# Performance work log

Hardware: AMD Instinct MI355X
Metric: run time of the kernel (lower is better)

## Reference

```python
import jax, jax.numpy as jnp
import numpy as np

N = 5000
NFEAT = 512
NHID = 64
NHEADS = 8
NCLASS = 40
ALPHA = 0.2  # leaky relu slope
NEG_INF = -9e15


def setup_inputs() -> dict:
    key = jax.random.key(0)
    ks = jax.random.split(key, 12)
    x = jax.random.normal(ks[0], (N, NFEAT), dtype=jnp.float32)
    # binary adjacency, ~32 avg degree, with self loops
    adj = (jax.random.uniform(ks[1], (N, N)) < (32.0 / N)).astype(jnp.float32)
    adj = jnp.maximum(adj, jnp.eye(N, dtype=jnp.float32))
    s = 1.0 / np.sqrt(NFEAT)
    W_h = jax.random.uniform(ks[2], (NHEADS, NFEAT, NHID), minval=-s, maxval=s, dtype=jnp.float32)
    a_h = jax.random.uniform(ks[3], (NHEADS, 2 * NHID), minval=-s, maxval=s, dtype=jnp.float32)
    s2 = 1.0 / np.sqrt(NHID * NHEADS)
    W_o = jax.random.uniform(ks[4], (NHID * NHEADS, NHID), minval=-s2, maxval=s2, dtype=jnp.float32)
    a_o = jax.random.uniform(ks[5], (2 * NHID,), minval=-s2, maxval=s2, dtype=jnp.float32)
    s3 = 1.0 / np.sqrt(NHID)
    fc1_w = jax.random.uniform(ks[6], (NHID, 200), minval=-s3, maxval=s3, dtype=jnp.float32)
    fc1_b = jax.random.uniform(ks[7], (200,), minval=-s3, maxval=s3, dtype=jnp.float32)
    s4 = 1.0 / np.sqrt(200)
    fc2_w = jax.random.uniform(ks[8], (200, NCLASS), minval=-s4, maxval=s4, dtype=jnp.float32)
    fc2_b = jax.random.uniform(ks[9], (NCLASS,), minval=-s4, maxval=s4, dtype=jnp.float32)
    return {"x": x, "adj": adj, "W_h": W_h, "a_h": a_h, "W_o": W_o, "a_o": a_o,
            "fc1_w": fc1_w, "fc1_b": fc1_b, "fc2_w": fc2_w, "fc2_b": fc2_b}


def _masked_attention(e, adj):
    # e: [..., N, N]; mask where adj == 0, then row softmax
    e = jnp.where(adj > 0, e, NEG_INF)
    return jax.nn.softmax(e, axis=-1)


def reference(x, adj, W_h, a_h, W_o, a_o, fc1_w, fc1_b, fc2_w, fc2_b):
    # ---- multi-head GAT layer (concat=True), eval mode (dropout off) ----
    Wh = jnp.einsum('nf,hfo->hno', x, W_h)                 # [H, N, nhid]
    f1 = jnp.einsum('hno,ho->hn', Wh, a_h[:, :NHID])       # [H, N]
    f2 = jnp.einsum('hno,ho->hn', Wh, a_h[:, NHID:])       # [H, N]
    e = jax.nn.leaky_relu(f1[:, :, None] + f2[:, None, :], ALPHA)  # [H, N, N]
    att = _masked_attention(e, adj[None, :, :])
    h = jnp.einsum('hnm,hmo->hno', att, Wh)                # [H, N, nhid]
    h1 = jax.nn.elu(h).transpose(1, 0, 2).reshape(N, NHEADS * NHID)  # concat heads

    # ---- output GAT layer (concat=False) ----
    Wh2 = h1 @ W_o                                         # [N, nhid]
    g1 = Wh2 @ a_o[:NHID]                                  # [N]
    g2 = Wh2 @ a_o[NHID:]                                  # [N]
    e2 = jax.nn.leaky_relu(g1[:, None] + g2[None, :], ALPHA)
    att2 = _masked_attention(e2, adj)
    h2 = att2 @ Wh2                                        # [N, nhid]

    # ---- MLP head ----
    h3 = jax.nn.elu(h2 @ fc1_w + fc1_b)
    return h3 @ fc2_w + fc2_b                              # [N, nclass]
```

## Files before the change

### kernel.cpp

```cpp
#include <hip/hip_runtime.h>

typedef unsigned short u16;
typedef unsigned int u32;
typedef unsigned long long u64;
typedef __bf16 bf16_t;
typedef __bf16 bf16x8 __attribute__((ext_vector_type(8)));
typedef float f32x4 __attribute__((ext_vector_type(4)));
typedef u32 u32x4 __attribute__((ext_vector_type(4)));

#define NN 5000
#define NF 512
#define NH 64
#define HEADS 8
#define NCLS 40
#define CAP 128
#define LRELU 0.2f

#define CVT_BIG 320
#define CVT_GRID (CVT_BIG + 8)
#define BM_BLKS 1250
#define G1_BLKS (79 * HEADS)

__device__ __forceinline__ bool adj_is_bf16(const void* adj) {
    return ((*(const u32*)adj) & 0xFFFFu) != 0u;
}
__device__ __forceinline__ u16 rne_bf16(float f) {
    u32 u = __float_as_uint(f);
    u += 0x7FFFu + ((u >> 16) & 1u);
    return (u16)(u >> 16);
}
__device__ __forceinline__ float up_bf16(u16 h) {
    return __uint_as_float((u32)h << 16);
}
__device__ __forceinline__ u32x4 ntload4(const void* p, int idx) {
    return __builtin_nontemporal_load(((const u32x4*)p) + idx);
}

__global__ __launch_bounds__(256) void cvt(const void* __restrict__ x, const void* __restrict__ W_h,
                                           const void* __restrict__ adj,
                                           const void* a_h, const void* W_o, const void* a_o,
                                           const void* f1w, const void* f1b,
                                           const void* f2w, const void* f2b,
                                           u16* __restrict__ xc, u16* __restrict__ whc,
                                           float* a_hc, float* W_oc, float* a_oc,
                                           float* f1wc, float* f1bc, float* f2wc, float* f2bc) {
    const bool isb = adj_is_bf16(adj);
    const int b = blockIdx.x;
    if (b < CVT_BIG) {
        const int X4 = NN * NF / 4;
        const int T4 = X4 + HEADS * NF * NH / 4;
        for (int i = b * 256 + threadIdx.x; i < T4; i += CVT_BIG * 256) {
            if (i < X4) {
                ushort4 o;
                if (isb) {
                    o = ((const ushort4*)x)[i];
                } else {
                    u32x4 vv = ntload4(x, i);
                    o.x = rne_bf16(__uint_as_float(vv[0])); o.y = rne_bf16(__uint_as_float(vv[1]));
                    o.z = rne_bf16(__uint_as_float(vv[2])); o.w = rne_bf16(__uint_as_float(vv[3]));
                }
                ((ushort4*)xc)[i] = o;
            } else {
                const int iw = i - X4;
                u16 q[4];
                if (isb) {
                    ushort4 vv = ((const ushort4*)W_h)[iw];
                    q[0] = vv.x; q[1] = vv.y; q[2] = vv.z; q[3] = vv.w;
                } else {
                    u32x4 vv = ntload4(W_h, iw);
                    q[0] = rne_bf16(__uint_as_float(vv[0])); q[1] = rne_bf16(__uint_as_float(vv[1]));
                    q[2] = rne_bf16(__uint_as_float(vv[2])); q[3] = rne_bf16(__uint_as_float(vv[3]));
                }
                const int e0 = iw * 4;
                const int h = e0 >> 15;
                const int rem = e0 & 32767;
                const int f = rem >> 6, o0 = rem & 63;
                const int base = (h * 16 + (f >> 5)) * 2048 + ((f >> 3) & 3) * 128 + (f & 7);
                #pragma unroll
                for (int k = 0; k < 4; ++k) {
                    const int o = o0 + k;
                    whc[base + (o >> 4) * 512 + (o & 15) * 8] = q[k];
                }
            }
        }
    } else {
        const int s0 = HEADS * 2 * NH, s1 = HEADS * NH * NH, s2 = 2 * NH,
                  s3 = NH * 200, s4 = 200, s5 = 200 * NCLS, s6 = NCLS;
        const int total = s0 + s1 + s2 + s3 + s4 + s5 + s6;
        for (int i = (b - CVT_BIG) * 256 + threadIdx.x; i < total; i += 8 * 256) {
            const void* src; float* dst; int off = i;
            if (off < s0) { src = a_h; dst = a_hc; }
            else if ((off -= s0) < s1) { src = W_o;  dst = W_oc; }
            else if ((off -= s1) < s2) { src = a_o;  dst = a_oc; }
            else if ((off -= s2) < s3) { src = f1w;  dst = f1wc; }
            else if ((off -= s3) < s4) { src = f1b;  dst = f1bc; }
            else if ((off -= s4) < s5) { src = f2w;  dst = f2wc; }
            else { off -= s5;           src = f2b;  dst = f2bc; }
            dst[off] = isb ? up_bf16(((const u16*)src)[off]) : ((const float*)src)[off];
        }
    }
}

__global__ __launch_bounds__(256) void gemm1_f(const bf16_t* __restrict__ x,
                                               const bf16_t* __restrict__ Wf,
                                               const float* __restrict__ a_h,
                                               const void* __restrict__ adj,
                                               int* __restrict__ nbr, int* __restrict__ deg,
                                               float* __restrict__ Wh,
                                               float* __restrict__ f1,
                                               float* __restrict__ f2) {
    const int lane = threadIdx.x & 63;
    const int wid  = threadIdx.x >> 6;
    const int b = blockIdx.x;

    if (b >= G1_BLKS) {
        const bool isb = adj_is_bf16(adj);
        const int r = (b - G1_BLKS) * 4 + wid;
        u64 my0 = 0ull, my1 = 0ull;
        if (!isb) {
            const float* row = (const float*)adj + (size_t)r * NN;
            #pragma unroll
            for (int pass = 0; pass < 2; ++pass) {
                u32x4 v[10];
                #pragma unroll
                for (int k = 0; k < 10; ++k) {
                    int c = (pass * 10 + k) * 64 + lane;
                    v[k] = (c < 1250) ? ntload4(row, c) : (u32x4){0u, 0u, 0u, 0u};
                }
                #pragma unroll
                for (int k = 0; k < 10; ++k) {
                    int i = pass * 10 + k;
                    #pragma unroll
                    for (int j = 0; j < 4; ++j) {
                        u64 m = __ballot(v[k][j] != 0u);
                        int w = i * 4 + j;
                        if (w == lane)      my0 = m;
                        if (w == lane + 64) my1 = m;
                    }
                }
            }
        } else {
            const u16* row = (const u16*)adj + (size_t)r * NN;
            u32x4 v[10];
            #pragma unroll
            for (int k = 0; k < 10; ++k) {
                int c = k * 64 + lane;
                v[k] = (c < 625) ? ntload4(row, c) : (u32x4){0u, 0u, 0u, 0u};
            }
            #pragma unroll
            for (int k = 0; k < 10; ++k) {
                #pragma unroll
                for (int j = 0; j < 4; ++j) {
                    u64 mlo = __ballot((v[k][j] & 0xFFFFu) != 0u);
                    u64 mhi = __ballot((v[k][j] >> 16) != 0u);
                    int wl = k * 8 + 2 * j, wh = wl + 1;
                    if (wl == lane)      my0 = mlo;
                    if (wl == lane + 64) my1 = mlo;
                    if (wh == lane)      my0 = mhi;
                    if (wh == lane + 64) my1 = mhi;
                }
            }
        }
        int* nrow = nbr + (size_t)r * CAP;
        int pc = __popcll(my0);
        int scan = pc;
        #pragma unroll
        for (int o = 1; o < 64; o <<= 1) {
            int t2 = __shfl_up(scan, o);
            if (lane >= o) scan += t2;
        }
        int off = scan - pc;
        {
            const int w = lane;
            u64 mw = my0;
            while (mw) {
                int bb = __ffsll(mw) - 1;
                mw &= mw - 1;
                int elem = !isb ? ((w >> 2) * 64 + bb) * 4 + (w & 3)
                                : ((w >> 3) * 64 + bb) * 8 + (w & 7);
                if (off < CAP) nrow[off] = elem;
                ++off;
            }
        }
        const int base = __shfl(scan, 63);
        int pc1 = __popcll(my1);
        int scan1 = pc1;
        #pragma unroll
        for (int o = 1; o < 64; o <<= 1) {
            int t2 = __shfl_up(scan1, o);
            if (lane >= o) scan1 += t2;
        }
        int off1 = base + scan1 - pc1;
        {
            const int w = lane + 64;
            u64 mw = my1;
            while (mw) {
                int bb = __ffsll(mw) - 1;
                mw &= mw - 1;
                int elem = !isb ? ((w >> 2) * 64 + bb) * 4 + (w & 3)
                                : ((w >> 3) * 64 + bb) * 8 + (w & 7);
                if (off1 < CAP) nrow[off1] = elem;
                ++off1;
            }
        }
        const int total = base + __shfl(scan1, 63);
        if (lane == 0) deg[r] = total < CAP ? total : CAP;
        return;
    }

    const int rg = b % 79;
    const int h  = b / 79;
    const int quad = lane >> 4;
    const int lr   = lane & 15;
    const int kq   = quad * 8;
    const int nCol = wid * 16 + lr;
    __shared__ float f1s[4][64], f2s[4][64];

    const bf16_t* Bf = Wf + (size_t)h * (16 * 2048) + threadIdx.x * 8;
    bf16x8 bfrag[16];
    #pragma unroll
    for (int s = 0; s < 16; ++s) bfrag[s] = *(const bf16x8*)(Bf + s * 2048);

    const float a1c = a_h[h * 128 + nCol];
    const float a2c = a_h[h * 128 + NH + nCol];

    for (int t = 0; t < 4; ++t) {
        const int rb = rg * 64 + t * 16;
        int row  = rb + lr;
        int rowc = row < NN ? row : NN - 1;
        const bf16_t* xp = x + (size_t)rowc * NF + kq;
        f32x4 acc = {0.f, 0.f, 0.f, 0.f};
        #pragma unroll
        for (int s = 0; s < 16; ++s) {
            bf16x8 a = *(const bf16x8*)(xp + s * 32);
            acc = __builtin_amdgcn_mfma_f32_16x16x32_bf16(a, bfrag[s], acc, 0, 0, 0);
        }
        #pragma unroll
        for (int r = 0; r < 4; ++r) {
            int gr = rb + quad * 4 + r;
            if (gr < NN) Wh[(size_t)gr * (HEADS * NH) + h * NH + nCol] = acc[r];
            float p1 = acc[r] * a1c, p2 = acc[r] * a2c;
            #pragma unroll
            for (int o = 8; o; o >>= 1) { p1 += __shfl_xor(p1, o); p2 += __shfl_xor(p2, o); }
            if (lr == 0) { f1s[wid][t * 16 + quad * 4 + r] = p1; f2s[wid][t * 16 + quad * 4 + r] = p2; }
        }
    }
    __syncthreads();
    if (wid == 0) {
        int gr = rg * 64 + lane;
        if (gr < NN) {
            f1[h * NN + gr] = f1s[0][lane] + f1s[1][lane] + f1s[2][lane] + f1s[3][lane];
            f2[h * NN + gr] = f2s[0][lane] + f2s[1][lane] + f2s[2][lane] + f2s[3][lane];
        }
    }
}

__global__ __launch_bounds__(256) void agg1f(const int* __restrict__ nbr,
                                             const int* __restrict__ deg,
                                             const float* __restrict__ Wh,
                                             const float* __restrict__ f1,
                                             const float* __restrict__ f2,
                                             float* __restrict__ h1) {
    const int lane = threadIdx.x & 63;
    const int wid  = threadIdx.x >> 6;
    const int n = blockIdx.x;
    __shared__ int s_nbr[CAP];
    __shared__ float s_p[8][CAP];
    const int d = deg[n];
    for (int i = threadIdx.x; i < d; i += 256) s_nbr[i] = nbr[(size_t)n * CAP + i];
    __syncthreads();

    const int ha = wid, hb = wid + 4;
    const int nb0 = (lane < d) ? s_nbr[lane] : 0;
    const int nb1 = (lane + 64 < d) ? s_nbr[lane + 64] : 0;
    const float f10 = f1[ha * NN + n], f11 = f1[hb * NN + n];
    const float* f2ha = f2 + (size_t)ha * NN;
    const float* f2hb = f2 + (size_t)hb * NN;

    float e00 = -INFINITY, e01 = -INFINITY, e10 = -INFINITY, e11 = -INFINITY;
    if (lane < d) {
        float a = f10 + f2ha[nb0]; e00 = a > 0.f ? a : LRELU * a;
        float b = f11 + f2hb[nb0]; e10 = b > 0.f ? b : LRELU * b;
    }
    if (lane + 64 < d) {
        float a = f10 + f2ha[nb1]; e01 = a > 0.f ? a : LRELU * a;
        float b = f11 + f2hb[nb1]; e11 = b > 0.f ? b : LRELU * b;
    }
    float mx0 = fmaxf(e00, e01), mx1 = fmaxf(e10, e11);
    #pragma unroll
    for (int o = 32; o; o >>= 1) {
        mx0 = fmaxf(mx0, __shfl_xor(mx0, o));
        mx1 = fmaxf(mx1, __shfl_xor(mx1, o));
    }
    float p00 = lane < d ? expf(e00 - mx0) : 0.f;
    float p01 = lane + 64 < d ? expf(e01 - mx0) : 0.f;
    float p10 = lane < d ? expf(e10 - mx1) : 0.f;
    float p11 = lane + 64 < d ? expf(e11 - mx1) : 0.f;
    float sm0 = p00 + p01, sm1 = p10 + p11;
    #pragma unroll
    for (int o = 32; o; o >>= 1) { sm0 += __shfl_xor(sm0, o); sm1 += __shfl_xor(sm1, o); }

    const float i0 = 1.f / sm0, i1 = 1.f / sm1;
    s_p[ha][lane] = p00 * i0; s_p[ha][lane + 64] = p01 * i0;
    s_p[hb][lane] = p10 * i1; s_p[hb][lane + 64] = p11 * i1;
    __syncthreads();

    const float* ap = s_p[2 * wid + (lane >> 5)];
    const float* wp = Wh + wid * 128 + 2 * lane;
    float A0x = 0.f, A0y = 0.f, A1x = 0.f, A1y = 0.f;
    float A2x = 0.f, A2y = 0.f, A3x = 0.f, A3y = 0.f;
    int j = 0;
    for (; j + 8 <= d; j += 8) {
        #pragma unroll
        for (int u = 0; u < 8; ++u) {
            const float2 v = *(const float2*)(wp + (size_t)s_nbr[j + u] * (HEADS * NH));
            const float a = ap[j + u];
            if ((u & 3) == 0)      { A0x += a * v.x; A0y += a * v.y; }
            else if ((u & 3) == 1) { A1x += a * v.x; A1y += a * v.y; }
            else if ((u & 3) == 2) { A2x += a * v.x; A2y += a * v.y; }
            else                   { A3x += a * v.x; A3y += a * v.y; }
        }
    }
    for (; j < d; ++j) {
        const float2 v = *(const float2*)(wp + (size_t)s_nbr[j] * (HEADS * NH));
        const float a = ap[j];
        A0x += a * v.x; A0y += a * v.y;
    }
    float hx = A0x + A1x + A2x + A3x;
    float hy = A0y + A1y + A2y + A3y;
    hx = hx > 0.f ? hx : expf(hx) - 1.f;
    hy = hy > 0.f ? hy : expf(hy) - 1.f;
    *(float2*)(h1 + (size_t)n * (HEADS * NH) + wid * 128 + 2 * lane) = make_float2(hx, hy);
}

__global__ __launch_bounds__(256) void gemm2_4(const float* __restrict__ h1,
                                               const float* __restrict__ W_o,
                                               const float* __restrict__ a_o,
                                               float* __restrict__ Wh2,
                                               float* __restrict__ g1,
                                               float* __restrict__ g2) {
    const int t = threadIdx.x;
    const int n0 = blockIdx.x * 4;
    __shared__ float sh[4 * 512];
    __shared__ float ps[4][4][64];
    const float4* src = (const float4*)(h1 + (size_t)n0 * 512);
    ((float4*)sh)[t]       = src[t];
    ((float4*)sh)[t + 256] = src[t + 256];
    __syncthreads();
    const int o = t & 63, part = t >> 6;
    float a0 = 0.f, a1 = 0.f, a2 = 0.f, a3 = 0.f;
    const float* wo = W_o + part * 128 * 64 + o;
    const float* s0 = sh + part * 128;
    #pragma unroll 4
    for (int f = 0; f < 128; ++f) {
        float w = wo[f * 64];
        a0 += s0[f] * w; a1 += s0[512 + f] * w; a2 += s0[1024 + f] * w; a3 += s0[1536 + f] * w;
    }
    ps[part][0][o] = a0; ps[part][1][o] = a1; ps[part][2][o] = a2; ps[part][3][o] = a3;
    __syncthreads();
    const int nd = t >> 6;
    float w2 = ps[0][nd][o] + ps[1][nd][o] + ps[2][nd][o] + ps[3][nd][o];
    Wh2[(size_t)(n0 + nd) * 64 + o] = w2;
    float p1 = w2 * a_o[o], p2 = w2 * a_o[64 + o];
    #pragma unroll
    for (int s = 32; s; s >>= 1) { p1 += __shfl_xor(p1, s); p2 += __shfl_xor(p2, s); }
    if (o == 0) { g1[n0 + nd] = p1; g2[n0 + nd] = p2; }
}

__global__ __launch_bounds__(256) void agg2_mlp(const float* __restrict__ Wh2,
                                                const float* __restrict__ g1,
                                                const float* __restrict__ g2,
                                                const int* __restrict__ nbr,
                                                const int* __restrict__ deg,
                                                const float* __restrict__ fc1_w,
                                                const float* __restrict__ fc1_b,
                                                const float* __restrict__ fc2_w,
                                                const float* __restrict__ fc2_b,
                                                float* __restrict__ out) {
    const int lane = threadIdx.x & 63;
    const int wid  = threadIdx.x >> 6;
    const int t = threadIdx.x;
    const int n0 = blockIdx.x * 4;
    const int n = n0 + wid;
    __shared__ float s_alpha[4][CAP];
    __shared__ int   s_nbr[4][CAP];
    __shared__ float s_h2[4][NH];
    __shared__ float s_h3[4][200];
    __shared__ float ps2[2][4][NCLS];
    const int d = deg[n];
    const int* nb = nbr + (size_t)n * CAP;
    const float gn = g1[n];

    float mx = -INFINITY;
    for (int j = lane; j < d; j += 64) {
        int m = nb[j];
        s_nbr[wid][j] = m;
        float e = gn + g2[m];
        e = e > 0.f ? e : LRELU * e;
        s_alpha[wid][j] = e;
        mx = fmaxf(mx, e);
    }
    #pragma unroll
    for (int o = 32; o; o >>= 1) mx = fmaxf(mx, __shfl_xor(mx, o));
    float sm = 0.f;
    for (int j = lane; j < d; j += 64) {
        float p = expf(s_alpha[wid][j] - mx);
        s_alpha[wid][j] = p;
        sm += p;
    }
    #pragma unroll
    for (int o = 32; o; o >>= 1) sm += __shfl_xor(sm, o);

    float acc0 = 0.f, acc1 = 0.f, acc2 = 0.f, acc3 = 0.f;
    int j = 0;
    for (; j + 4 <= d; j += 4) {
        acc0 += s_alpha[wid][j]     * Wh2[(size_t)s_nbr[wid][j]     * NH + lane];
        acc1 += s_alpha[wid][j + 1] * Wh2[(size_t)s_nbr[wid][j + 1] * NH + lane];
        acc2 += s_alpha[wid][j + 2] * Wh2[(size_t)s_nbr[wid][j + 2] * NH + lane];
        acc3 += s_alpha[wid][j + 3] * Wh2[(size_t)s_nbr[wid][j + 3] * NH + lane];
    }
    for (; j < d; ++j) acc0 += s_alpha[wid][j] * Wh2[(size_t)s_nbr[wid][j] * NH + lane];
    s_h2[wid][lane] = (acc0 + acc1 + acc2 + acc3) / sm;
    __syncthreads();

    if (t < 200) {
        float b0 = 0.f, b1 = 0.f, b2 = 0.f, b3 = 0.f;
        #pragma unroll 4
        for (int f = 0; f < NH; ++f) {
            float w = fc1_w[f * 200 + t];
            b0 += s_h2[0][f] * w; b1 += s_h2[1][f] * w; b2 += s_h2[2][f] * w; b3 += s_h2[3][f] * w;
        }
        float bb = fc1_b[t];
        b0 += bb; b1 += bb; b2 += bb; b3 += bb;
        s_h3[0][t] = b0 > 0.f ? b0 : expf(b0) - 1.f;
        s_h3[1][t] = b1 > 0.f ? b1 : expf(b1) - 1.f;
        s_h3[2][t] = b2 > 0.f ? b2 : expf(b2) - 1.f;
        s_h3[3][t] = b3 > 0.f ? b3 : expf(b3) - 1.f;
    }
    __syncthreads();

    if (t < 80) {
        const int o = t % 40, fh = t / 40;
        float c0 = 0.f, c1 = 0.f, c2 = 0.f, c3 = 0.f;
        #pragma unroll 4
        for (int f = fh * 100; f < fh * 100 + 100; ++f) {
            float w = fc2_w[f * NCLS + o];
            c0 += s_h3[0][f] * w; c1 += s_h3[1][f] * w; c2 += s_h3[2][f] * w; c3 += s_h3[3][f] * w;
        }
        ps2[fh][0][o] = c0; ps2[fh][1][o] = c1; ps2[fh][2][o] = c2; ps2[fh][3][o] = c3;
    }
    __syncthreads();
    if (t < 160) {
        const int nd = t / 40, o = t % 40;
        out[(size_t)(n0 + nd) * NCLS + o] = ps2[0][nd][o] + ps2[1][nd][o] + fc2_b[o];
    }
}

extern "C" void kernel_launch(void* const* d_in, const int* in_sizes, int n_in,
                              void* d_out, int out_size, void* d_ws, size_t ws_size,
                              hipStream_t stream) {
    const void* x     = d_in[0];
    const void* adj   = d_in[1];
    const void* W_h   = d_in[2];
    const void* a_h   = d_in[3];
    const void* W_o   = d_in[4];
    const void* a_o   = d_in[5];
    const void* fc1_w = d_in[6];
    const void* fc1_b = d_in[7];
    const void* fc2_w = d_in[8];
    const void* fc2_b = d_in[9];
    float* out = (float*)d_out;

    char* ws = (char*)d_ws;
    int*   nbr   = (int*)(ws + 0);
    int*   deg   = (int*)(ws + 2560000);
    float* Wh    = (float*)(ws + 2580000);
    float* f1    = (float*)(ws + 12820000);
    float* f2    = (float*)(ws + 12980000);
    float* h1    = (float*)(ws + 13140000);
    float* Wh2   = (float*)(ws + 23380000);
    float* g1    = (float*)(ws + 24660000);
    float* g2    = (float*)(ws + 24680000);
    u16*   xc    = (u16*)(ws + 24700000);
    u16*   whc   = (u16*)(ws + 29820000);
    float* a_hc  = (float*)(ws + 30344288);
    float* W_oc  = (float*)(ws + 30348384);
    float* a_oc  = (float*)(ws + 30479456);
    float* f1wc  = (float*)(ws + 30479968);
    float* f1bc  = (float*)(ws + 30531168);
    float* f2wc  = (float*)(ws + 30531968);
    float* f2bc  = (float*)(ws + 30563968);

    cvt<<<CVT_GRID, 256, 0, stream>>>(x, W_h, adj, a_h, W_o, a_o,
                                      fc1_w, fc1_b, fc2_w, fc2_b,
                                      xc, whc, a_hc, W_oc, a_oc,
                                      f1wc, f1bc, f2wc, f2bc);
    gemm1_f<<<G1_BLKS + BM_BLKS, 256, 0, stream>>>((const bf16_t*)xc, (const bf16_t*)whc,
                                                   a_hc, adj, nbr, deg, Wh, f1, f2);
    agg1f<<<NN, 256, 0, stream>>>(nbr, deg, Wh, f1, f2, h1);
    gemm2_4<<<NN / 4, 256, 0, stream>>>(h1, W_oc, a_oc, Wh2, g1, g2);
    agg2_mlp<<<NN / 4, 256, 0, stream>>>(Wh2, g1, g2, nbr, deg,
                                         f1wc, f1bc, f2wc, f2bc, out);
}
```

Measured before the change: 268.9 us.

## Fuse input conversion kernel into gemm1, converting x and W_h on the fly

Removes the separate cvt kernel that converted x and W_h to bf16 and repacked W_h into an MFMA-friendly layout. gemm1 now reads fp32 (or bf16) x and W_h directly and converts in registers. The small parameter conversions move into extra blocks of the same launch. Adjacency-scan blocks are reordered to come first. This saves one kernel launch and a write-plus-reread of the converted x, at the cost of strided scalar loads for the W_h fragments and twice the x read bytes when x is fp32.

New measurement: 286.8 us. 1.07x slower.

```diff
diff --git a/kernel.cpp b/kernel.cpp
--- a/kernel.cpp
+++ b/kernel.cpp
@@ -5,6 +5,7 @@
 typedef unsigned long long u64;
 typedef __bf16 bf16_t;
 typedef __bf16 bf16x8 __attribute__((ext_vector_type(8)));
+typedef u16 u16x8 __attribute__((ext_vector_type(8)));
 typedef float f32x4 __attribute__((ext_vector_type(4)));
 typedef u32 u32x4 __attribute__((ext_vector_type(4)));
 
@@ -16,106 +17,46 @@
 #define CAP 128
 #define LRELU 0.2f
 
-#define CVT_BIG 320
-#define CVT_GRID (CVT_BIG + 8)
 #define BM_BLKS 1250
 #define G1_BLKS (79 * HEADS)
+#define PRM_BLKS 8
+#define K1_GRID (BM_BLKS + G1_BLKS + PRM_BLKS)
 
 __device__ __forceinline__ bool adj_is_bf16(const void* adj) {
     return ((*(const u32*)adj) & 0xFFFFu) != 0u;
 }
-__device__ __forceinline__ u16 rne_bf16(float f) {
-    u32 u = __float_as_uint(f);
-    u += 0x7FFFu + ((u >> 16) & 1u);
-    return (u16)(u >> 16);
-}
 __device__ __forceinline__ float up_bf16(u16 h) {
     return __uint_as_float((u32)h << 16);
 }
+__device__ __forceinline__ float in_f32(const void* p, int idx, bool isb) {
+    return isb ? up_bf16(((const u16*)p)[idx]) : ((const float*)p)[idx];
+}
 __device__ __forceinline__ u32x4 ntload4(const void* p, int idx) {
     return __builtin_nontemporal_load(((const u32x4*)p) + idx);
 }
-
-__global__ __launch_bounds__(256) void cvt(const void* __restrict__ x, const void* __restrict__ W_h,
-                                           const void* __restrict__ adj,
-                                           const void* a_h, const void* W_o, const void* a_o,
-                                           const void* f1w, const void* f1b,
-                                           const void* f2w, const void* f2b,
-                                           u16* __restrict__ xc, u16* __restrict__ whc,
-                                           float* a_hc, float* W_oc, float* a_oc,
-                                           float* f1wc, float* f1bc, float* f2wc, float* f2bc) {
-    const bool isb = adj_is_bf16(adj);
-    const int b = blockIdx.x;
-    if (b < CVT_BIG) {
-        const int X4 = NN * NF / 4;
-        const int T4 = X4 + HEADS * NF * NH / 4;
-        for (int i = b * 256 + threadIdx.x; i < T4; i += CVT_BIG * 256) {
-            if (i < X4) {
-                ushort4 o;
-                if (isb) {
-                    o = ((const ushort4*)x)[i];
-                } else {
-                    u32x4 vv = ntload4(x, i);
-                    o.x = rne_bf16(__uint_as_float(vv[0])); o.y = rne_bf16(__uint_as_float(vv[1]));
-                    o.z = rne_bf16(__uint_as_float(vv[2])); o.w = rne_bf16(__uint_as_float(vv[3]));
-                }
-                ((ushort4*)xc)[i] = o;
-            } else {
-                const int iw = i - X4;
-                u16 q[4];
-                if (isb) {
-                    ushort4 vv = ((const ushort4*)W_h)[iw];
-                    q[0] = vv.x; q[1] = vv.y; q[2] = vv.z; q[3] = vv.w;
-                } else {
-                    u32x4 vv = ntload4(W_h, iw);
-                    q[0] = rne_bf16(__uint_as_float(vv[0])); q[1] = rne_bf16(__uint_as_float(vv[1]));
-                    q[2] = rne_bf16(__uint_as_float(vv[2])); q[3] = rne_bf16(__uint_as_float(vv[3]));
-                }
-                const int e0 = iw * 4;
-                const int h = e0 >> 15;
-                const int rem = e0 & 32767;
-                const int f = rem >> 6, o0 = rem & 63;
-                const int base = (h * 16 + (f >> 5)) * 2048 + ((f >> 3) & 3) * 128 + (f & 7);
-                #pragma unroll
-                for (int k = 0; k < 4; ++k) {
-                    const int o = o0 + k;
-                    whc[base + (o >> 4) * 512 + (o & 15) * 8] = q[k];
-                }
-            }
-        }
-    } else {
-        const int s0 = HEADS * 2 * NH, s1 = HEADS * NH * NH, s2 = 2 * NH,
-                  s3 = NH * 200, s4 = 200, s5 = 200 * NCLS, s6 = NCLS;
-        const int total = s0 + s1 + s2 + s3 + s4 + s5 + s6;
-        for (int i = (b - CVT_BIG) * 256 + threadIdx.x; i < total; i += 8 * 256) {
-            const void* src; float* dst; int off = i;
-            if (off < s0) { src = a_h; dst = a_hc; }
-            else if ((off -= s0) < s1) { src = W_o;  dst = W_oc; }
-            else if ((off -= s1) < s2) { src = a_o;  dst = a_oc; }
-            else if ((off -= s2) < s3) { src = f1w;  dst = f1wc; }
-            else if ((off -= s3) < s4) { src = f1b;  dst = f1bc; }
-            else if ((off -= s4) < s5) { src = f2w;  dst = f2wc; }
-            else { off -= s5;           src = f2b;  dst = f2bc; }
-            dst[off] = isb ? up_bf16(((const u16*)src)[off]) : ((const float*)src)[off];
-        }
-    }
-}
-
-__global__ __launch_bounds__(256) void gemm1_f(const bf16_t* __restrict__ x,
-                                               const bf16_t* __restrict__ Wf,
-                                               const float* __restrict__ a_h,
+union U8cast { u16x8 u; bf16x8 b; };
+
+__global__ __launch_bounds__(256) void gemm1_f(const void* __restrict__ x,
+                                               const void* __restrict__ W_h,
+                                               const void* __restrict__ a_h,
                                                const void* __restrict__ adj,
+                                               const void* W_o, const void* a_o,
+                                               const void* f1w, const void* f1b,
+                                               const void* f2w, const void* f2b,
                                                int* __restrict__ nbr, int* __restrict__ deg,
                                                float* __restrict__ Wh,
                                                float* __restrict__ f1,
-                                               float* __restrict__ f2) {
+                                               float* __restrict__ f2,
+                                               float* W_oc, float* a_oc,
+                                               float* f1wc, float* f1bc,
+                                               float* f2wc, float* f2bc) {
+    const bool isb = adj_is_bf16(adj);
     const int lane = threadIdx.x & 63;
     const int wid  = threadIdx.x >> 6;
     const int b = blockIdx.x;
 
-    if (b >= G1_BLKS) {
-        const bool isb = adj_is_bf16(adj);
-        const int r = (b - G1_BLKS) * 4 + wid;
+    if (b < BM_BLKS) {
+        const int r = b * 4 + wid;
         u64 my0 = 0ull, my1 = 0ull;
         if (!isb) {
             const float* row = (const float*)adj + (size_t)r * NN;
@@ -208,32 +149,80 @@
         return;
     }
 
-    const int rg = b % 79;
-    const int h  = b / 79;
+    if (b >= BM_BLKS + G1_BLKS) {
+        const int s1 = HEADS * NH * NH, s2 = 2 * NH,
+                  s3 = NH * 200, s4 = 200, s5 = 200 * NCLS, s6 = NCLS;
+        const int total = s1 + s2 + s3 + s4 + s5 + s6;
+        const int pb = b - (BM_BLKS + G1_BLKS);
+        for (int i = pb * 256 + threadIdx.x; i < total; i += PRM_BLKS * 256) {
+            const void* src; float* dst; int off = i;
+            if (off < s1) { src = W_o;  dst = W_oc; }
+            else if ((off -= s1) < s2) { src = a_o;  dst = a_oc; }
+            else if ((off -= s2) < s3) { src = f1w;  dst = f1wc; }
+            else if ((off -= s3) < s4) { src = f1b;  dst = f1bc; }
+            else if ((off -= s4) < s5) { src = f2w;  dst = f2wc; }
+            else { off -= s5;           src = f2b;  dst = f2bc; }
+            dst[off] = isb ? up_bf16(((const u16*)src)[off]) : ((const float*)src)[off];
+        }
+        return;
+    }
+
+    const int g = b - BM_BLKS;
+    const int rg = g % 79;
+    const int h  = g / 79;
     const int quad = lane >> 4;
     const int lr   = lane & 15;
     const int kq   = quad * 8;
     const int nCol = wid * 16 + lr;
     __shared__ float f1s[4][64], f2s[4][64];
 
-    const bf16_t* Bf = Wf + (size_t)h * (16 * 2048) + threadIdx.x * 8;
     bf16x8 bfrag[16];
-    #pragma unroll
-    for (int s = 0; s < 16; ++s) bfrag[s] = *(const bf16x8*)(Bf + s * 2048);
-
-    const float a1c = a_h[h * 128 + nCol];
-    const float a2c = a_h[h * 128 + NH + nCol];
+    if (!isb) {
+        const float* Bh = (const float*)W_h + (size_t)h * NF * NH;
+        #pragma unroll
+        for (int s = 0; s < 16; ++s) {
+            bf16x8 bb;
+            #pragma unroll
+            for (int j = 0; j < 8; ++j) bb[j] = (bf16_t)Bh[(s * 32 + kq + j) * NH + nCol];
+            bfrag[s] = bb;
+        }
+    } else {
+        const u16* Bh = (const u16*)W_h + (size_t)h * NF * NH;
+        #pragma unroll
+        for (int s = 0; s < 16; ++s) {
+            U8cast cc;
+            #pragma unroll
+            for (int j = 0; j < 8; ++j) cc.u[j] = Bh[(s * 32 + kq + j) * NH + nCol];
+            bfrag[s] = cc.b;
+        }
+    }
+    const float a1c = in_f32(a_h, h * 128 + nCol, isb);
+    const float a2c = in_f32(a_h, h * 128 + NH + nCol, isb);
 
     for (int t = 0; t < 4; ++t) {
         const int rb = rg * 64 + t * 16;
         int row  = rb + lr;
         int rowc = row < NN ? row : NN - 1;
-        const bf16_t* xp = x + (size_t)rowc * NF + kq;
         f32x4 acc = {0.f, 0.f, 0.f, 0.f};
-        #pragma unroll
-        for (int s = 0; s < 16; ++s) {
-            bf16x8 a = *(const bf16x8*)(xp + s * 32);
-            acc = __builtin_amdgcn_mfma_f32_16x16x32_bf16(a, bfrag[s], acc, 0, 0, 0);
+        if (!isb) {
+            const float* xp = (const float*)x + (size_t)rowc * NF + kq;
+            #pragma unroll
+            for (int s = 0; s < 16; ++s) {
+                float4 lo = *(const float4*)(xp + s * 32);
+                float4 hi = *(const float4*)(xp + s * 32 + 4);
+                bf16x8 a;
+                a[0] = (bf16_t)lo.x; a[1] = (bf16_t)lo.y; a[2] = (bf16_t)lo.z; a[3] = (bf16_t)lo.w;
+                a[4] = (bf16_t)hi.x; a[5] = (bf16_t)hi.y; a[6] = (bf16_t)hi.z; a[7] = (bf16_t)hi.w;
+                acc = __builtin_amdgcn_mfma_f32_16x16x32_bf16(a, bfrag[s], acc, 0, 0, 0);
+            }
+        } else {
+            const u16* xp = (const u16*)x + (size_t)rowc * NF + kq;
+            #pragma unroll
+            for (int s = 0; s < 16; ++s) {
+                U8cast cc;
+                cc.u = *(const u16x8*)(xp + s * 32);
+                acc = __builtin_amdgcn_mfma_f32_16x16x32_bf16(cc.b, bfrag[s], acc, 0, 0, 0);
+            }
         }
         #pragma unroll
         for (int r = 0; r < 4; ++r) {
@@ -481,22 +470,17 @@
     float* Wh2   = (float*)(ws + 23380000);
     float* g1    = (float*)(ws + 24660000);
     float* g2    = (float*)(ws + 24680000);
-    u16*   xc    = (u16*)(ws + 24700000);
-    u16*   whc   = (u16*)(ws + 29820000);
-    float* a_hc  = (float*)(ws + 30344288);
-    float* W_oc  = (float*)(ws + 30348384);
-    float* a_oc  = (float*)(ws + 30479456);
-    float* f1wc  = (float*)(ws + 30479968);
-    float* f1bc  = (float*)(ws + 30531168);
-    float* f2wc  = (float*)(ws + 30531968);
-    float* f2bc  = (float*)(ws + 30563968);
-
-    cvt<<<CVT_GRID, 256, 0, stream>>>(x, W_h, adj, a_h, W_o, a_o,
-                                      fc1_w, fc1_b, fc2_w, fc2_b,
-                                      xc, whc, a_hc, W_oc, a_oc,
-                                      f1wc, f1bc, f2wc, f2bc);
-    gemm1_f<<<G1_BLKS + BM_BLKS, 256, 0, stream>>>((const bf16_t*)xc, (const bf16_t*)whc,
-                                                   a_hc, adj, nbr, deg, Wh, f1, f2);
+    float* W_oc  = (float*)(ws + 24700000);
+    float* a_oc  = (float*)(ws + 24831072);
+    float* f1wc  = (float*)(ws + 24831584);
+    float* f1bc  = (float*)(ws + 24882784);
+    float* f2wc  = (float*)(ws + 24883584);
+    float* f2bc  = (float*)(ws + 24915584);
+
+    gemm1_f<<<K1_GRID, 256, 0, stream>>>(x, W_h, a_h, adj,
+                                         W_o, a_o, fc1_w, fc1_b, fc2_w, fc2_b,
+                                         nbr, deg, Wh, f1, f2,
+                                         W_oc, a_oc, f1wc, f1bc, f2wc, f2bc);
     agg1f<<<NN, 256, 0, stream>>>(nbr, deg, Wh, f1, f2, h1);
     gemm2_4<<<NN / 4, 256, 0, stream>>>(h1, W_oc, a_oc, Wh2, g1, g2);
     agg2_mlp<<<NN / 4, 256, 0, stream>>>(Wh2, g1, g2, nbr, deg,
```
